# Performance work log

Measured on AMD Instinct MI355X. Metric: run time of the kernel, lower is better.

The kernel has to match this reference:

```python
import jax, jax.numpy as jnp
import numpy as np

B, N, DM, DK, DV, H, DFF, K = 16, 1024, 512, 256, 256, 4, 2048, 20
EPS = 1e-5


def _layer_norm(x, g, b):
    mu = jnp.mean(x, axis=-1, keepdims=True)
    var = jnp.mean((x - mu) ** 2, axis=-1, keepdims=True)
    return (x - mu) * jax.lax.rsqrt(var + EPS) * g + b


def setup_inputs() -> dict:
    key = jax.random.key(0)
    ks = jax.random.split(key, 12)
    s = 0.02
    return {
        "vertices": jax.random.normal(ks[0], (B, N, 3), jnp.float32),
        "F": jax.random.normal(ks[1], (B, N, DM), jnp.float32),
        "Wq": jax.random.normal(ks[2], (DM, H * DK), jnp.float32) * s,
        "bq": jnp.zeros((H * DK,), jnp.float32),
        "Wk": jax.random.normal(ks[3], (DM, H * DK), jnp.float32) * s,
        "bk": jnp.zeros((H * DK,), jnp.float32),
        "Wv": jax.random.normal(ks[4], (DM, H * DV), jnp.float32) * s,
        "bv": jnp.zeros((H * DV,), jnp.float32),
        "Wo": jax.random.normal(ks[5], (H * DV, DM), jnp.float32) * s,
        "bo": jnp.zeros((DM,), jnp.float32),
        "ln1_g": jnp.ones((DM,), jnp.float32),
        "ln1_b": jnp.zeros((DM,), jnp.float32),
        "W1": jax.random.normal(ks[6], (DM, DFF), jnp.float32) * s,
        "b1": jnp.zeros((DFF,), jnp.float32),
        "W2": jax.random.normal(ks[7], (DFF, DM), jnp.float32) * s,
        "b2": jnp.zeros((DM,), jnp.float32),
        "ln2_g": jnp.ones((DM,), jnp.float32),
        "ln2_b": jnp.zeros((DM,), jnp.float32),
    }


def _knn_mask(vertices):
    x2 = jnp.sum(vertices * vertices, axis=-1)
    dist = x2[:, :, None] + x2[:, None, :] - 2.0 * jnp.einsum("bnc,bmc->bnm", vertices, vertices)
    # torch.topk(dist, k, dim=1, largest=False) then transpose -> [B, dst, k] of src indices
    _, idx = jax.lax.top_k(-jnp.swapaxes(dist, 1, 2), K)  # [B, N, K]
    counts = jnp.sum(jax.nn.one_hot(idx, N, dtype=jnp.int32), axis=-2)  # [B, N, N]
    return counts < 1  # True = masked out


def reference(vertices, F, Wq, bq, Wk, bk, Wv, bv, Wo, bo, ln1_g, ln1_b,
              W1, b1, W2, b2, ln2_g, ln2_b):
    mask = _knn_mask(vertices)  # [B, N, N] bool; shared across heads

    q = (F @ Wq + bq).reshape(B, N, H, DK).transpose(0, 2, 1, 3)  # [B,H,N,DK]
    k = (F @ Wk + bk).reshape(B, N, H, DK).transpose(0, 2, 1, 3)
    v = (F @ Wv + bv).reshape(B, N, H, DV).transpose(0, 2, 1, 3)

    att = jnp.einsum("bhnd,bhmd->bhnm", q, k) / jnp.sqrt(jnp.float32(DK))
    att = jnp.where(mask[:, None, :, :], -jnp.inf, att)
    att = jax.nn.softmax(att, axis=-1)

    out = jnp.einsum("bhnm,bhmd->bhnd", att, v)
    out = out.transpose(0, 2, 1, 3).reshape(B, N, H * DV) @ Wo + bo

    x = _layer_norm(F + out, ln1_g, ln1_b)  # residual + LN (mha)
    ff = jax.nn.relu(x @ W1 + b1) @ W2 + b2  # position-wise FFN
    return _layer_norm(x + ff, ln2_g, ln2_b)
```

## Files before the change

### kernel.cpp

```cpp
#include <hip/hip_runtime.h>
#include <stdint.h>

typedef uint16_t u16;
typedef __bf16 bf16x8 __attribute__((ext_vector_type(8)));
typedef float f32x4 __attribute__((ext_vector_type(4)));

#define DEV static __device__ __forceinline__

DEV float bfbits_lo(uint32_t w) { union { uint32_t i; float f; } v; v.i = w << 16; return v.f; }
DEV float bfbits_hi(uint32_t w) { union { uint32_t i; float f; } v; v.i = w & 0xffff0000u; return v.f; }
DEV u16 f2bf(float f) {
    union { float f; uint32_t i; } v; v.f = f;
    uint32_t x = v.i;
    uint32_t r = (x + 0x7fffu + ((x >> 16) & 1u)) >> 16;
    return (u16)r;
}


__global__ __launch_bounds__(256) void prep_kernel(
    const float* __restrict__ verts, const float* __restrict__ F,
    const float* __restrict__ Wq, const float* __restrict__ Wk,
    const float* __restrict__ Wv, const float* __restrict__ Wo,
    const float* __restrict__ W1, const float* __restrict__ W2,
    const float* __restrict__ bq, const float* __restrict__ bk,
    const float* __restrict__ bv,
    u16* __restrict__ WqkvT, u16* __restrict__ WoT,
    u16* __restrict__ W1T, u16* __restrict__ W2T,
    float* __restrict__ bqkv, u16* __restrict__ Fb, int* __restrict__ nbr) {
    int blk = blockIdx.x;
    int tid = threadIdx.x;
    if (blk < 4096) {
        const float* in; u16* outp; int K, Nsrc, NB, noff, t = blk;
        if (t < 512) { in = Wq; outp = WqkvT; K = 512; Nsrc = 1024; NB = 3072; noff = 0; }
        else if (t < 1024) { t -= 512; in = Wk; outp = WqkvT; K = 512; Nsrc = 1024; NB = 3072; noff = 1024; }
        else if (t < 1536) { t -= 1024; in = Wv; outp = WqkvT; K = 512; Nsrc = 1024; NB = 3072; noff = 2048; }
        else if (t < 2048) { t -= 1536; in = Wo; outp = WoT; K = 1024; Nsrc = 512; NB = 512; noff = 0; }
        else if (t < 3072) { t -= 2048; in = W1; outp = W1T; K = 512; Nsrc = 2048; NB = 2048; noff = 0; }
        else { t -= 3072; in = W2; outp = W2T; K = 2048; Nsrc = 512; NB = 512; noff = 0; }
        int tilesX = Nsrc >> 5;
        int bx = t % tilesX, by = t / tilesX;
        int x0 = bx * 32, y0 = by * 32;
        __shared__ float tile[32][33];
        int tx = tid & 31, ty = tid >> 5;
#pragma unroll
        for (int r = 0; r < 4; r++) {
            int y = y0 + ty + r * 8;
            tile[ty + r * 8][tx] = in[(size_t)y * Nsrc + x0 + tx];
        }
        __syncthreads();
#pragma unroll
        for (int r = 0; r < 4; r++) {
            int n = x0 + ty + r * 8;
            int k = y0 + tx;
            outp[(((size_t)(k >> 3) * NB + noff + n) << 3) + (k & 7)] = f2bf(tile[tx][ty + r * 8]);
        }
    } else if (blk < 8192) {
        int gi = (blk - 4096) * 256 + tid;
        int row = gi >> 6, p = gi & 63;
        const float4* src = (const float4*)(F + (size_t)row * 512 + p * 8);
        float4 a = src[0], c = src[1];
        uint32_t w0 = f2bf(a.x) | ((uint32_t)f2bf(a.y) << 16);
        uint32_t w1 = f2bf(a.z) | ((uint32_t)f2bf(a.w) << 16);
        uint32_t w2 = f2bf(c.x) | ((uint32_t)f2bf(c.y) << 16);
        uint32_t w3 = f2bf(c.z) | ((uint32_t)f2bf(c.w) << 16);
        ((uint4*)Fb)[(size_t)p * 16384 + row] = make_uint4(w0, w1, w2, w3);
    } else if (blk < 8204) {
        int i = (blk - 8192) * 256 + tid;
        if (i < 1024) bqkv[i] = bq[i];
        else if (i < 2048) bqkv[i] = bk[i - 1024];
        else if (i < 3072) bqkv[i] = bv[i - 2048];
    } else {
        int wv = (blk - 8204) * 4 + (tid >> 6);
        int l = tid & 63;
        int b = wv >> 10, n = wv & 1023;
        const float* vb = verts + (size_t)b * 1024 * 3;
        float qx = vb[n * 3 + 0], qy = vb[n * 3 + 1], qz = vb[n * 3 + 2];
        float q2 = qx * qx + qy * qy + qz * qz;
        float d[16];
#pragma unroll
        for (int t = 0; t < 16; t++) {
            int p = l + 64 * t;
            float px = vb[p * 3 + 0], py = vb[p * 3 + 1], pz = vb[p * 3 + 2];
            float p2 = px * px + py * py + pz * pz;
            float dot = qx * px + qy * py + qz * pz;
            d[t] = q2 + p2 - 2.f * dot;
        }
        int* outp = nbr + (size_t)wv * 20;
        for (int it = 0; it < 20; it++) {
            float dm = d[0]; int im = 0;
#pragma unroll
            for (int t = 1; t < 16; t++) { if (d[t] < dm) { dm = d[t]; im = t; } }
            int g = im * 64 + l;
#pragma unroll
            for (int off = 32; off >= 1; off >>= 1) {
                float od = __shfl_xor(dm, off);
                int og = __shfl_xor(g, off);
                if (od < dm || (od == dm && og < g)) { dm = od; g = og; }
            }
            int wl = g & 63, wt = g >> 6;
            if (l == wl) {
#pragma unroll
                for (int t = 0; t < 16; t++) if (t == wt) d[t] = 3.4e38f;
            }
            if (l == 0) outp[it] = g;
        }
    }
}

template <int EPI>
__global__ __launch_bounds__(256) void gemm_bt(const u16* __restrict__ A,
                                               const u16* __restrict__ BT,
                                               const float* __restrict__ bias,
                                               u16* __restrict__ Cb,
                                               float* __restrict__ Cf,
                                               float* __restrict__ Cf2,
                                               int M, int N, int Klen,
                                               int MA, int NB, int Koff) {
    __shared__ __align__(16) u16 As0[4096], As1[4096];
    __shared__ __align__(16) u16 Bs0[4096], Bs1[4096];
    int tid = threadIdx.x;
    int id = blockIdx.y * gridDim.x + blockIdx.x;
    int by = id % gridDim.y, bx = id / gridDim.y;
    int m0 = by * 128, n0 = bx * 128;
    int kz = blockIdx.z;
    const uint4* A4 = (const uint4*)A + (size_t)kz * (Koff >> 3) * MA;
    const uint4* B4 = (const uint4*)BT + (size_t)kz * (Koff >> 3) * NB;
    int w = tid >> 6, l = tid & 63;
    int wr = w >> 1, wc = w & 1, quad = l >> 4, ln = l & 15;
    int qA = tid >> 7, rA = tid & 127;
    const uint4* pA0 = A4 + (size_t)qA * MA + m0 + rA;
    const uint4* pA1 = pA0 + 2 * (size_t)MA;
    const uint4* pB0 = B4 + (size_t)qA * NB + n0 + rA;
    const uint4* pB1 = pB0 + 2 * (size_t)NB;

    f32x4 acc[4][4];
#pragma unroll
    for (int i = 0; i < 4; i++)
#pragma unroll
        for (int j = 0; j < 4; j++) acc[i][j] = (f32x4){0.f, 0.f, 0.f, 0.f};

    uint4 a00, a01, b00, b01;
    uint4 a10, a11, b10, b11;

#define ISSUE0(ko) do { size_t kq = (size_t)((ko) >> 3);                             \
        a00 = pA0[kq * MA]; a01 = pA1[kq * MA];                                      \
        b00 = pB0[kq * NB]; b01 = pB1[kq * NB]; } while (0)
#define ISSUE1(ko) do { size_t kq = (size_t)((ko) >> 3);                             \
        a10 = pA0[kq * MA]; a11 = pA1[kq * MA];                                      \
        b10 = pB0[kq * NB]; b11 = pB1[kq * NB]; } while (0)
#define WRITE0() do { *(uint4*)((char*)As0 + tid * 16) = a00; *(uint4*)((char*)As0 + (tid + 256) * 16) = a01; \
                      *(uint4*)((char*)Bs0 + tid * 16) = b00; *(uint4*)((char*)Bs0 + (tid + 256) * 16) = b01; } while (0)
#define WRITE1() do { *(uint4*)((char*)As1 + tid * 16) = a10; *(uint4*)((char*)As1 + (tid + 256) * 16) = a11; \
                      *(uint4*)((char*)Bs1 + tid * 16) = b10; *(uint4*)((char*)Bs1 + (tid + 256) * 16) = b11; } while (0)
#define COMPUTE(Asb, Bsb) do {                                                            \
        const bf16x8* Av = (const bf16x8*)(Asb);                                          \
        const bf16x8* Bv = (const bf16x8*)(Bsb);                                          \
        bf16x8 af[4], bfr[4];                                                             \
        _Pragma("unroll")                                                                 \
        for (int i = 0; i < 4; i++) af[i] = Av[quad * 128 + wr * 64 + i * 16 + ln];       \
        _Pragma("unroll")                                                                 \
        for (int j = 0; j < 4; j++) bfr[j] = Bv[quad * 128 + wc * 64 + j * 16 + ln];      \
        _Pragma("unroll")                                                                 \
        for (int i = 0; i < 4; i++)                                                       \
            _Pragma("unroll")                                                             \
            for (int j = 0; j < 4; j++)                                                   \
                acc[i][j] = __builtin_amdgcn_mfma_f32_16x16x32_bf16(af[i], bfr[j], acc[i][j], 0, 0, 0); \
    } while (0)
#define LGKM_BARRIER() do { asm volatile("s_waitcnt lgkmcnt(0)" ::: "memory"); \
                            __builtin_amdgcn_s_barrier(); } while (0)

    int nIter = Klen >> 5;
    ISSUE0(0);
    ISSUE1(32);
    WRITE0();
    LGKM_BARRIER();
    for (int kt = 0; kt < nIter; kt += 2) {
        if (kt + 2 < nIter) ISSUE0((kt + 2) * 32);
        COMPUTE(As0, Bs0);
        WRITE1();
        LGKM_BARRIER();
        if (kt + 3 < nIter) ISSUE1((kt + 3) * 32);
        COMPUTE(As1, Bs1);
        if (kt + 2 < nIter) {
            WRITE0();
            LGKM_BARRIER();
        }
    }
#undef ISSUE0
#undef ISSUE1
#undef WRITE0
#undef WRITE1
#undef COMPUTE
#undef LGKM_BARRIER

    float* Cfz = (EPI == 3) ? (kz ? Cf2 : Cf) : Cf;
#pragma unroll
    for (int i = 0; i < 4; i++) {
        int row_base = m0 + wr * 64 + i * 16 + quad * 4;
#pragma unroll
        for (int j = 0; j < 4; j++) {
            int col = n0 + wc * 64 + j * 16 + ln;
            float bb = (EPI == 3) ? 0.f : bias[col];
#pragma unroll
            for (int r = 0; r < 4; r++) {
                int row = row_base + r;
                float v = acc[i][j][r] + bb;
                if (EPI == 0) Cb[(size_t)row * N + col] = f2bf(v);
                else if (EPI == 1)
                    Cb[(((size_t)(col >> 3) * M + row) << 3) + (col & 7)] = f2bf(v > 0.f ? v : 0.f);
                else Cfz[(size_t)row * N + col] = v;
            }
        }
    }
}

__global__ __launch_bounds__(256) void attn_kernel(const u16* __restrict__ QKV,
                                                   const int* __restrict__ nbr,
                                                   u16* __restrict__ outA) {
    int tid = threadIdx.x;
    int wv = blockIdx.x * 4 + (tid >> 6);
    int l = tid & 63;
    int h = l >> 4, sx = l & 15;
    int bbase = (wv >> 10) << 10;

    int nv = 0;
    if (l < 20) nv = nbr[(size_t)wv * 20 + l];

    const uint32_t* qp = (const uint32_t*)(QKV + (size_t)wv * 3072 + h * 256 + sx * 16);
    uint32_t qw[8];
    *(uint4*)(qw) = *(const uint4*)qp;
    *(uint4*)(qw + 4) = *(const uint4*)(qp + 4);
    float qf[16];
#pragma unroll
    for (int i = 0; i < 8; i++) { qf[2 * i] = bfbits_lo(qw[i]); qf[2 * i + 1] = bfbits_hi(qw[i]); }

    float wj[20];
#pragma unroll
    for (int j = 0; j < 20; j++) {
        int m = __shfl(nv, j);
        const uint32_t* kp = (const uint32_t*)(QKV + (size_t)(bbase + m) * 3072 + 1024 + h * 256 + sx * 16);
        uint32_t kw[8];
        *(uint4*)(kw) = *(const uint4*)kp;
        *(uint4*)(kw + 4) = *(const uint4*)(kp + 4);
        float acc = 0.f;
#pragma unroll
        for (int i = 0; i < 8; i++) {
            acc += qf[2 * i] * bfbits_lo(kw[i]);
            acc += qf[2 * i + 1] * bfbits_hi(kw[i]);
        }
#pragma unroll
        for (int off = 1; off < 16; off <<= 1) acc += __shfl_xor(acc, off);
        wj[j] = acc * 0.0625f;
    }
    float mx = wj[0];
#pragma unroll
    for (int j = 1; j < 20; j++) mx = fmaxf(mx, wj[j]);
    float ssum = 0.f;
#pragma unroll
    for (int j = 0; j < 20; j++) { wj[j] = __expf(wj[j] - mx); ssum += wj[j]; }
    float inv = 1.f / ssum;

    float o[16];
#pragma unroll
    for (int i = 0; i < 16; i++) o[i] = 0.f;
#pragma unroll
    for (int j = 0; j < 20; j++) {
        int m = __shfl(nv, j);
        const uint32_t* vp = (const uint32_t*)(QKV + (size_t)(bbase + m) * 3072 + 2048 + h * 256 + sx * 16);
        uint32_t vw[8];
        *(uint4*)(vw) = *(const uint4*)vp;
        *(uint4*)(vw + 4) = *(const uint4*)(vp + 4);
        float ww = wj[j] * inv;
#pragma unroll
        for (int i = 0; i < 8; i++) {
            o[2 * i] += ww * bfbits_lo(vw[i]);
            o[2 * i + 1] += ww * bfbits_hi(vw[i]);
        }
    }
    uint32_t ow[8];
#pragma unroll
    for (int i = 0; i < 8; i++) ow[i] = f2bf(o[2 * i]) | ((uint32_t)f2bf(o[2 * i + 1]) << 16);
    size_t slot = (size_t)(h * 32 + sx * 2) * 16384 + wv;
    ((uint4*)outA)[slot] = make_uint4(ow[0], ow[1], ow[2], ow[3]);
    ((uint4*)outA)[slot + 16384] = make_uint4(ow[4], ow[5], ow[6], ow[7]);
}

template <int WB>
__global__ __launch_bounds__(256) void ln12p_kernel(const float* __restrict__ P0,
                                                    const float* __restrict__ P1,
                                                    const float* __restrict__ res,
                                                    const float* __restrict__ biasv,
                                                    const float* __restrict__ g,
                                                    const float* __restrict__ bparm,
                                                    float* __restrict__ Yf,
                                                    u16* __restrict__ Yb) {
    int tid = threadIdx.x;
    int row = blockIdx.x * 4 + (tid >> 6);
    int l = tid & 63;
    size_t base = (size_t)row * 512;
    const float4* p0 = (const float4*)(P0 + base) + l * 2;
    const float4* p1 = (const float4*)(P1 + base) + l * 2;
    const float4* rr = (const float4*)(res + base) + l * 2;
    const float4* bv = (const float4*)biasv + l * 2;
    float xs[8];
#pragma unroll
    for (int h = 0; h < 2; h++) {
        float4 a = p0[h], b = p1[h], c = rr[h], d = bv[h];
        xs[4 * h + 0] = a.x + b.x + c.x + d.x;
        xs[4 * h + 1] = a.y + b.y + c.y + d.y;
        xs[4 * h + 2] = a.z + b.z + c.z + d.z;
        xs[4 * h + 3] = a.w + b.w + c.w + d.w;
    }
    float s = 0.f;
#pragma unroll
    for (int i = 0; i < 8; i++) s += xs[i];
#pragma unroll
    for (int off = 32; off >= 1; off >>= 1) s += __shfl_xor(s, off);
    float mu = s * (1.f / 512.f);
    float q = 0.f;
#pragma unroll
    for (int i = 0; i < 8; i++) { float dd = xs[i] - mu; q += dd * dd; }
#pragma unroll
    for (int off = 32; off >= 1; off >>= 1) q += __shfl_xor(q, off);
    float var = q * (1.f / 512.f);
    float rs = rsqrtf(var + 1e-5f);
    const float4* gp = (const float4*)g + l * 2;
    const float4* bp = (const float4*)bparm + l * 2;
    float4 g0 = gp[0], g1 = gp[1], b0 = bp[0], b1 = bp[1];
    float gg[8] = {g0.x, g0.y, g0.z, g0.w, g1.x, g1.y, g1.z, g1.w};
    float bbv[8] = {b0.x, b0.y, b0.z, b0.w, b1.x, b1.y, b1.z, b1.w};
    float y[8];
#pragma unroll
    for (int i = 0; i < 8; i++) y[i] = (xs[i] - mu) * rs * gg[i] + bbv[i];
    float4* yo = (float4*)(Yf + base) + l * 2;
    yo[0] = make_float4(y[0], y[1], y[2], y[3]);
    yo[1] = make_float4(y[4], y[5], y[6], y[7]);
    if (WB) {
        uint32_t w0 = f2bf(y[0]) | ((uint32_t)f2bf(y[1]) << 16);
        uint32_t w1 = f2bf(y[2]) | ((uint32_t)f2bf(y[3]) << 16);
        uint32_t w2 = f2bf(y[4]) | ((uint32_t)f2bf(y[5]) << 16);
        uint32_t w3 = f2bf(y[6]) | ((uint32_t)f2bf(y[7]) << 16);
        ((uint4*)Yb)[(size_t)l * 16384 + row] = make_uint4(w0, w1, w2, w3);
    }
}

extern "C" void kernel_launch(void* const* d_in, const int* in_sizes, int n_in,
                              void* d_out, int out_size, void* d_ws, size_t ws_size,
                              hipStream_t stream) {
    const float* verts = (const float*)d_in[0];
    const float* F = (const float*)d_in[1];
    const float* Wq = (const float*)d_in[2];
    const float* bq = (const float*)d_in[3];
    const float* Wk = (const float*)d_in[4];
    const float* bk = (const float*)d_in[5];
    const float* Wv = (const float*)d_in[6];
    const float* bv = (const float*)d_in[7];
    const float* Wo = (const float*)d_in[8];
    const float* bo = (const float*)d_in[9];
    const float* ln1g = (const float*)d_in[10];
    const float* ln1b = (const float*)d_in[11];
    const float* W1 = (const float*)d_in[12];
    const float* b1 = (const float*)d_in[13];
    const float* W2 = (const float*)d_in[14];
    const float* b2 = (const float*)d_in[15];
    const float* ln2g = (const float*)d_in[16];
    const float* ln2b = (const float*)d_in[17];
    float* out = (float*)d_out;

    char* ws = (char*)d_ws;
    u16* QKV = (u16*)(ws);
    float* Q0 = (float*)(ws);
    float* Q1 = (float*)(ws + 33554432);
    u16* Hb = (u16*)(ws);
    float* P1 = (float*)(ws + 67108864);
    u16* ATT = (u16*)(ws + 100663296);
    u16* xb = ATT;
    float* P0 = (float*)(ws + 100663296);
    u16* Fb = (u16*)(ws + 134217728);
    float* X32 = (float*)(ws + 134217728);
    char* wsw = ws + 167772160;
    u16* WqkvT = (u16*)(wsw);
    u16* WoT = (u16*)(wsw + 3145728);
    u16* W1T = (u16*)(wsw + 4194304);
    u16* W2T = (u16*)(wsw + 6291456);
    float* bqkv = (float*)(wsw + 8388608);
    int* nbr = (int*)(wsw + 8404992);

    prep_kernel<<<12300, 256, 0, stream>>>(verts, F, Wq, Wk, Wv, Wo, W1, W2,
                                           bq, bk, bv, WqkvT, WoT, W1T, W2T,
                                           bqkv, Fb, nbr);
    gemm_bt<0><<<dim3(24, 128, 1), 256, 0, stream>>>(Fb, WqkvT, bqkv, QKV, nullptr, nullptr,
                                                     16384, 3072, 512, 16384, 3072, 0);
    attn_kernel<<<4096, 256, 0, stream>>>(QKV, nbr, ATT);
    gemm_bt<3><<<dim3(4, 128, 2), 256, 0, stream>>>(ATT, WoT, nullptr, nullptr, Q0, Q1,
                                                    16384, 512, 512, 16384, 512, 512);
    ln12p_kernel<1><<<4096, 256, 0, stream>>>(Q0, Q1, F, bo, ln1g, ln1b, X32, xb);
    gemm_bt<1><<<dim3(16, 128, 1), 256, 0, stream>>>(xb, W1T, b1, Hb, nullptr, nullptr,
                                                     16384, 2048, 512, 16384, 2048, 0);
    gemm_bt<3><<<dim3(4, 128, 2), 256, 0, stream>>>(Hb, W2T, nullptr, nullptr, P0, P1,
                                                    16384, 512, 1024, 16384, 512, 1024);
    ln12p_kernel<0><<<4096, 256, 0, stream>>>(P0, P1, X32, b2, ln2g, ln2b, out, nullptr);
}
```

Before: 562.5 us.

## Fuse attention score and value passes, use DPP reductions and block swizzle

The attention kernel now reads each neighbour's K and V row together and builds the softmax numerator and output in a single loop. The old two passes, max pass and second gather of neighbour indices are gone, and normalisation happens once at the end. The 16-lane dot-product reduction uses DPP row-rotate and quad-perm moves instead of cross-lane shuffles. Blocks are remapped with a swizzle to change L2 locality of the neighbour gathers. Dropping the max subtraction risks exp overflow if scores grow large, and it depends on small score magnitudes.

```diff
diff --git a/kernel.cpp b/kernel.cpp
--- a/kernel.cpp
+++ b/kernel.cpp
@@ -14,6 +14,14 @@
     uint32_t x = v.i;
     uint32_t r = (x + 0x7fffu + ((x >> 16) & 1u)) >> 16;
     return (u16)r;
+}
+
+template <int CTRL>
+DEV float dpp_get(float x) {
+    union { float f; int i; } a, r;
+    a.f = x;
+    r.i = __builtin_amdgcn_update_dpp(0, a.i, CTRL, 0xf, 0xf, false);
+    return r.f;
 }
 
 
@@ -218,7 +226,9 @@
                                                    const int* __restrict__ nbr,
                                                    u16* __restrict__ outA) {
     int tid = threadIdx.x;
-    int wv = blockIdx.x * 4 + (tid >> 6);
+    int bid = blockIdx.x;
+    int swz = (bid & 7) * 512 + (bid >> 3);
+    int wv = swz * 4 + (tid >> 6);
     int l = tid & 63;
     int h = l >> 4, sx = l & 15;
     int bbase = (wv >> 10) << 10;
@@ -234,52 +244,44 @@
 #pragma unroll
     for (int i = 0; i < 8; i++) { qf[2 * i] = bfbits_lo(qw[i]); qf[2 * i + 1] = bfbits_hi(qw[i]); }
 
-    float wj[20];
+    float o[16];
+#pragma unroll
+    for (int i = 0; i < 16; i++) o[i] = 0.f;
+    float ssum = 0.f;
+
 #pragma unroll
     for (int j = 0; j < 20; j++) {
         int m = __shfl(nv, j);
-        const uint32_t* kp = (const uint32_t*)(QKV + (size_t)(bbase + m) * 3072 + 1024 + h * 256 + sx * 16);
-        uint32_t kw[8];
-        *(uint4*)(kw) = *(const uint4*)kp;
-        *(uint4*)(kw + 4) = *(const uint4*)(kp + 4);
-        float acc = 0.f;
+        const u16* kvrow = QKV + (size_t)(bbase + m) * 3072 + 1024 + h * 256 + sx * 16;
+        uint32_t kw[8], vw[8];
+        *(uint4*)(kw) = *(const uint4*)(kvrow);
+        *(uint4*)(kw + 4) = *(const uint4*)(kvrow + 8);
+        *(uint4*)(vw) = *(const uint4*)(kvrow + 1024);
+        *(uint4*)(vw + 4) = *(const uint4*)(kvrow + 1032);
+        float acc0 = 0.f, acc1 = 0.f;
 #pragma unroll
         for (int i = 0; i < 8; i++) {
-            acc += qf[2 * i] * bfbits_lo(kw[i]);
-            acc += qf[2 * i + 1] * bfbits_hi(kw[i]);
-        }
-#pragma unroll
-        for (int off = 1; off < 16; off <<= 1) acc += __shfl_xor(acc, off);
-        wj[j] = acc * 0.0625f;
-    }
-    float mx = wj[0];
-#pragma unroll
-    for (int j = 1; j < 20; j++) mx = fmaxf(mx, wj[j]);
-    float ssum = 0.f;
-#pragma unroll
-    for (int j = 0; j < 20; j++) { wj[j] = __expf(wj[j] - mx); ssum += wj[j]; }
+            acc0 += qf[2 * i] * bfbits_lo(kw[i]);
+            acc1 += qf[2 * i + 1] * bfbits_hi(kw[i]);
+        }
+        float acc = acc0 + acc1;
+        acc += dpp_get<0x124>(acc);
+        acc += dpp_get<0x128>(acc);
+        acc += dpp_get<0xB1>(acc);
+        acc += dpp_get<0x4E>(acc);
+        float e = __expf(acc * 0.0625f);
+        ssum += e;
+#pragma unroll
+        for (int i = 0; i < 8; i++) {
+            o[2 * i] += e * bfbits_lo(vw[i]);
+            o[2 * i + 1] += e * bfbits_hi(vw[i]);
+        }
+    }
     float inv = 1.f / ssum;
-
-    float o[16];
-#pragma unroll
-    for (int i = 0; i < 16; i++) o[i] = 0.f;
-#pragma unroll
-    for (int j = 0; j < 20; j++) {
-        int m = __shfl(nv, j);
-        const uint32_t* vp = (const uint32_t*)(QKV + (size_t)(bbase + m) * 3072 + 2048 + h * 256 + sx * 16);
-        uint32_t vw[8];
-        *(uint4*)(vw) = *(const uint4*)vp;
-        *(uint4*)(vw + 4) = *(const uint4*)(vp + 4);
-        float ww = wj[j] * inv;
-#pragma unroll
-        for (int i = 0; i < 8; i++) {
-            o[2 * i] += ww * bfbits_lo(vw[i]);
-            o[2 * i + 1] += ww * bfbits_hi(vw[i]);
-        }
-    }
     uint32_t ow[8];
 #pragma unroll
-    for (int i = 0; i < 8; i++) ow[i] = f2bf(o[2 * i]) | ((uint32_t)f2bf(o[2 * i + 1]) << 16);
+    for (int i = 0; i < 8; i++)
+        ow[i] = f2bf(o[2 * i] * inv) | ((uint32_t)f2bf(o[2 * i + 1] * inv) << 16);
     size_t slot = (size_t)(h * 32 + sx * 2) * 16384 + wv;
     ((uint4*)outA)[slot] = make_uint4(ow[0], ow[1], ow[2], ow[3]);
     ((uint4*)outA)[slot + 16384] = make_uint4(ow[4], ow[5], ow[6], ow[7]);
```

New measurement: 627.6 us. +11.6%, slower.
